# Optimization experiments

Hardware: AMD Instinct MI355X
Metric: run time of the kernel (lower is better)

## Reference

```python
import jax, jax.numpy as jnp
import numpy as np

HIDDEN = 128
N_LAYERS = 6
N_NODES = 50000
N_EDGES = 640000


def _glorot(key, shape):
    fan_in, fan_out = shape[0], shape[1]
    lim = (6.0 / (fan_in + fan_out)) ** 0.5
    return jax.random.uniform(key, shape, jnp.float32, -lim, lim)


def setup_inputs() -> dict:
    key = jax.random.key(0)
    ks = jax.random.split(key, 8)
    pos = jax.random.normal(ks[0], (N_NODES, 3), jnp.float32)
    edge_attr = jax.random.normal(ks[1], (N_EDGES, 3), jnp.float32)
    edge_index = jax.random.randint(ks[2], (2, N_EDGES), 0, N_NODES, jnp.int64)
    enc_w = _glorot(ks[3], (3, HIDDEN)); enc_b = jnp.zeros((HIDDEN,), jnp.float32)
    dec_w = _glorot(ks[4], (HIDDEN, 3)); dec_b = jnp.zeros((3,), jnp.float32)
    lk = jax.random.split(ks[5], 4 * N_LAYERS)
    edge_w1 = jnp.stack([_glorot(lk[4 * i + 0], (3 * HIDDEN, HIDDEN)) for i in range(N_LAYERS)])
    edge_w2 = jnp.stack([_glorot(lk[4 * i + 1], (HIDDEN, HIDDEN)) for i in range(N_LAYERS)])
    node_w1 = jnp.stack([_glorot(lk[4 * i + 2], (2 * HIDDEN, HIDDEN)) for i in range(N_LAYERS)])
    node_w2 = jnp.stack([_glorot(lk[4 * i + 3], (HIDDEN, HIDDEN)) for i in range(N_LAYERS)])
    edge_b1 = jnp.zeros((N_LAYERS, HIDDEN), jnp.float32)
    edge_b2 = jnp.zeros((N_LAYERS, HIDDEN), jnp.float32)
    node_b1 = jnp.zeros((N_LAYERS, HIDDEN), jnp.float32)
    node_b2 = jnp.zeros((N_LAYERS, HIDDEN), jnp.float32)
    return dict(pos=pos, edge_attr=edge_attr, edge_index=edge_index,
                enc_w=enc_w, enc_b=enc_b, dec_w=dec_w, dec_b=dec_b,
                edge_w1=edge_w1, edge_b1=edge_b1, edge_w2=edge_w2, edge_b2=edge_b2,
                node_w1=node_w1, node_b1=node_b1, node_w2=node_w2, node_b2=node_b2)


def _interaction(x, ef, src, dst, ew1, eb1, ew2, eb2, nw1, nb1, nw2, nb2, n_nodes):
    # message: concat(x_i=x[dst], x_j=x[src], edge_feature) -> edge MLP
    m = jnp.concatenate([x[dst], x[src], ef], axis=-1)            # [E, 3H]
    m = jax.nn.relu(m @ ew1 + eb1) @ ew2 + eb2                     # [E, H]
    # scatter-mean by target node
    sums = jax.ops.segment_sum(m, dst, num_segments=n_nodes)      # [N, H]
    cnt = jax.ops.segment_sum(jnp.ones((m.shape[0],), m.dtype), dst, num_segments=n_nodes)
    aggr = sums / jnp.maximum(cnt, 1.0)[:, None]
    node = jnp.concatenate([x, aggr], axis=-1)                     # [N, 2H]
    node = jax.nn.relu(node @ nw1 + nb1) @ nw2 + nb2               # [N, H]
    return x + node, ef + m


def reference(pos, edge_attr, edge_index, enc_w, enc_b, dec_w, dec_b,
              edge_w1, edge_b1, edge_w2, edge_b2,
              node_w1, node_b1, node_w2, node_b2):
    n_nodes = pos.shape[0]
    src = edge_index[0]
    dst = edge_index[1]
    x = jnp.zeros((n_nodes, HIDDEN), jnp.float32)
    ef = edge_attr @ enc_w + enc_b
    for i in range(N_LAYERS):
        x, ef = _interaction(x, ef, src, dst,
                             edge_w1[i], edge_b1[i], edge_w2[i], edge_b2[i],
                             node_w1[i], node_b1[i], node_w2[i], node_b2[i], n_nodes)
    out = x @ dec_w + dec_b                                        # [N, 3]
    # F.normalize(dim=1, eps=1e-12)
    norm = jnp.linalg.norm(out, axis=1, keepdims=True)
    return out / jnp.maximum(norm, 1e-12)
```

## Files before the change

### kernel.cpp

```cpp
#include <hip/hip_runtime.h>
#include <cstdint>

#define HIDDEN  128
#define NLAYERS 6
#define NNODES  50000
#define NEDGES  640000

typedef short short8 __attribute__((ext_vector_type(8)));
typedef float f32x4  __attribute__((ext_vector_type(4)));

__device__ __forceinline__ float bf2f(unsigned short u) {
    return __uint_as_float(((unsigned int)u) << 16);
}
__device__ __forceinline__ unsigned short f2bf(float f) {
    unsigned int u = __float_as_uint(f);
    unsigned int r = u + 0x7FFFu + ((u >> 16) & 1u);
    return (unsigned short)(r >> 16);
}
__device__ __forceinline__ unsigned int pack2(float a, float b) {
    return (unsigned int)f2bf(a) | ((unsigned int)f2bf(b) << 16);
}
__device__ __forceinline__ void unpack8(uint4 v, float* f) {
    f[0] = bf2f((unsigned short)(v.x & 0xffff)); f[1] = bf2f((unsigned short)(v.x >> 16));
    f[2] = bf2f((unsigned short)(v.y & 0xffff)); f[3] = bf2f((unsigned short)(v.y >> 16));
    f[4] = bf2f((unsigned short)(v.z & 0xffff)); f[5] = bf2f((unsigned short)(v.z >> 16));
    f[6] = bf2f((unsigned short)(v.w & 0xffff)); f[7] = bf2f((unsigned short)(v.w >> 16));
}

__global__ void detect_kernel(const int* __restrict__ ei, int* __restrict__ flag)
{
    int lane = threadIdx.x;
    int v = ei[2 * lane + 1];
    unsigned long long b = __ballot(v != 0);
    if (lane == 0) *flag = (b != 0ULL) ? 1 : 0;
}

__global__ void normidx_kernel(const int* __restrict__ ei, const int* __restrict__ flag,
                               int* __restrict__ s32, int* __restrict__ d32)
{
    int e = blockIdx.x * blockDim.x + threadIdx.x;
    if (e >= NEDGES) return;
    int s, d;
    if (*flag) { s = ei[e]; d = ei[NEDGES + e]; }
    else       { s = ei[2 * e]; d = ei[2 * (NEDGES + e)]; }
    s32[e] = min(max(s, 0), NNODES - 1);
    d32[e] = min(max(d, 0), NNODES - 1);
}

__global__ void degree_kernel(const int* __restrict__ dst, int* __restrict__ deg)
{
    int e = blockIdx.x * blockDim.x + threadIdx.x;
    if (e < NEDGES) atomicAdd(&deg[dst[e]], 1);
}

#define SCAN_T 1024
__global__ void scan_kernel(const int* __restrict__ deg, int* __restrict__ off,
                            int* __restrict__ cursor)
{
    __shared__ int part[SCAN_T];
    const int t = threadIdx.x;
    const int CH = (NNODES + SCAN_T - 1) / SCAN_T;
    const int base = t * CH;
    int s = 0;
    for (int i = 0; i < CH; ++i) {
        int idx = base + i;
        if (idx < NNODES) s += deg[idx];
    }
    part[t] = s;
    __syncthreads();
    for (int d = 1; d < SCAN_T; d <<= 1) {
        int v = (t >= d) ? part[t - d] : 0;
        __syncthreads();
        part[t] += v;
        __syncthreads();
    }
    int run = (t == 0) ? 0 : part[t - 1];
    for (int i = 0; i < CH; ++i) {
        int idx = base + i;
        if (idx < NNODES) {
            off[idx] = run;
            cursor[idx] = run;
            run += deg[idx];
        }
    }
    if (t == SCAN_T - 1) off[NNODES] = run;
}

__global__ void scatter_kernel(const int* __restrict__ s32, const int* __restrict__ d32,
                               int* __restrict__ cursor,
                               int* __restrict__ sp, int* __restrict__ dp, int* __restrict__ ep)
{
    int e = blockIdx.x * blockDim.x + threadIdx.x;
    if (e >= NEDGES) return;
    int d = d32[e];
    int p = atomicAdd(&cursor[d], 1);
    sp[p] = s32[e];
    dp[p] = d;
    ep[p] = e;
}

__global__ void transpose_kernel(const float* __restrict__ W, unsigned short* __restrict__ WT,
                                 int K, int N, int L)
{
    long idx = (long)blockIdx.x * 256 + threadIdx.x;
    long tot = (long)L * K * N;
    if (idx >= tot) return;
    int kn = (int)(idx % ((long)K * N));
    int l  = (int)(idx / ((long)K * N));
    int k = kn / N;
    int n = kn % N;
    WT[(long)l * K * N + (long)n * K + k] = f2bf(W[idx]);
}

__global__ void encode_kernel(const float* __restrict__ ea,
                              const float* __restrict__ w,
                              const float* __restrict__ b,
                              const int* __restrict__ ep,
                              unsigned short* __restrict__ ef)
{
    int idx = blockIdx.x * blockDim.x + threadIdx.x;
    int p = idx >> 5;
    if (p >= NEDGES) return;
    int e = ep[p];
    int j = (idx & 31) << 2;
    float a0 = ea[e * 3 + 0], a1 = ea[e * 3 + 1], a2 = ea[e * 3 + 2];
    float4 w0 = *(const float4*)(w + 0 * HIDDEN + j);
    float4 w1 = *(const float4*)(w + 1 * HIDDEN + j);
    float4 w2 = *(const float4*)(w + 2 * HIDDEN + j);
    float4 bb = *(const float4*)(b + j);
    ushort4 o;
    o.x = f2bf(fmaf(a0, w0.x, fmaf(a1, w1.x, fmaf(a2, w2.x, bb.x))));
    o.y = f2bf(fmaf(a0, w0.y, fmaf(a1, w1.y, fmaf(a2, w2.y, bb.y))));
    o.z = f2bf(fmaf(a0, w0.z, fmaf(a1, w1.z, fmaf(a2, w2.z, bb.z))));
    o.w = f2bf(fmaf(a0, w0.w, fmaf(a1, w1.w, fmaf(a2, w2.w, bb.w))));
    *(ushort4*)(ef + (long)p * HIDDEN + j) = o;
}

__global__ __launch_bounds__(256, 3)
void edge_layer_mfma(const unsigned short* __restrict__ Xa,
                     const unsigned short* __restrict__ Xb,
                     unsigned short* __restrict__ ef,
                     float* __restrict__ sums,
                     const int* __restrict__ sp,
                     const int* __restrict__ dp,
                     const unsigned short* __restrict__ W1T,
                     const float* __restrict__ b1,
                     const unsigned short* __restrict__ W2T,
                     const float* __restrict__ b2)
{
    __shared__ __align__(16) unsigned char buf[45056];
    unsigned short* As = (unsigned short*)buf;
    unsigned short* Hs = (unsigned short*)buf;
    unsigned short* Bs = (unsigned short*)(buf + 34816);
    __shared__ int dv[128];
    __shared__ int sv[128];

    const int tid = threadIdx.x;
    const long eb = (long)blockIdx.x * 128;
    if (tid < 128) dv[tid]       = dp[eb + tid];
    else           sv[tid - 128] = sp[eb + tid - 128];

    const int lane = tid & 63;
    const int wv   = tid >> 6;
    const int mn   = lane & 15;
    const int q    = lane >> 4;
    const int rr   = tid >> 1;
    const int o    = (tid & 1) << 4;
    const int bn   = tid >> 1;
    const int bk   = (tid & 1) << 4;

    __syncthreads();

    f32x4 acc[2][8];
#pragma unroll
    for (int h = 0; h < 2; ++h)
#pragma unroll
        for (int t = 0; t < 8; ++t) acc[h][t] = (f32x4)0.0f;

    uint4 pa0, pa1, pw0, pw1;
    {
        const unsigned short* epp = ef + (eb + rr) * HIDDEN + o;
        pa0 = *(const uint4*)epp;
        pa1 = *(const uint4*)(epp + 8);
        const unsigned short* wp = W1T + (long)bn * 384 + 256 + bk;
        pw0 = *(const uint4*)wp;
        pw1 = *(const uint4*)(wp + 8);
    }

    for (int c = 0; c < 4; ++c) {
        *(uint4*)&As[rr * 40 + o]     = pa0;
        *(uint4*)&As[rr * 40 + o + 8] = pa1;
        *(uint4*)&Bs[bn * 40 + bk]     = pw0;
        *(uint4*)&Bs[bn * 40 + bk + 8] = pw1;
        __syncthreads();

        if (c + 1 < 4) {
            const int cn = c + 1;
            const unsigned short* epp = ef + (eb + rr) * HIDDEN + (cn << 5) + o;
            pa0 = *(const uint4*)epp;
            pa1 = *(const uint4*)(epp + 8);
            const unsigned short* wp = W1T + (long)bn * 384 + 256 + (cn << 5) + bk;
            pw0 = *(const uint4*)wp;
            pw1 = *(const uint4*)(wp + 8);
        }

        short8 af0 = *(short8*)&As[(wv * 32 + mn) * 40 + (q << 3)];
        short8 af1 = *(short8*)&As[(wv * 32 + 16 + mn) * 40 + (q << 3)];
#pragma unroll
        for (int nt = 0; nt < 8; ++nt) {
            short8 bf = *(short8*)&Bs[(nt * 16 + mn) * 40 + (q << 3)];
            acc[0][nt] = __builtin_amdgcn_mfma_f32_16x16x32_bf16(af0, bf, acc[0][nt], 0, 0, 0);
            acc[1][nt] = __builtin_amdgcn_mfma_f32_16x16x32_bf16(af1, bf, acc[1][nt], 0, 0, 0);
        }
        __syncthreads();
    }

#pragma unroll
    for (int h = 0; h < 2; ++h)
#pragma unroll
        for (int r = 0; r < 4; ++r) {
            const int row = wv * 32 + h * 16 + q * 4 + r;
            const long ba = (long)dv[row] * HIDDEN;
            const long bb = (long)sv[row] * HIDDEN;
#pragma unroll
            for (int nt = 0; nt < 8; ++nt) {
                const int col = nt * 16 + mn;
                float add = bf2f(Xa[ba + col]) + bf2f(Xb[bb + col]) + b1[col];
                float hv = fmaxf(acc[h][nt][r] + add, 0.0f);
                Hs[row * 136 + col] = f2bf(hv);
            }
        }

    f32x4 acc2[2][8];
#pragma unroll
    for (int h = 0; h < 2; ++h)
#pragma unroll
        for (int t = 0; t < 8; ++t) acc2[h][t] = (f32x4)0.0f;
    {
        const unsigned short* wp = W2T + (long)bn * 128 + bk;
        pw0 = *(const uint4*)wp;
        pw1 = *(const uint4*)(wp + 8);
    }
    for (int c = 0; c < 4; ++c) {
        *(uint4*)&Bs[bn * 40 + bk]     = pw0;
        *(uint4*)&Bs[bn * 40 + bk + 8] = pw1;
        __syncthreads();
        if (c + 1 < 4) {
            const unsigned short* wp = W2T + (long)bn * 128 + ((c + 1) << 5) + bk;
            pw0 = *(const uint4*)wp;
            pw1 = *(const uint4*)(wp + 8);
        }
        short8 af0 = *(short8*)&Hs[(wv * 32 + mn) * 136 + (c << 5) + (q << 3)];
        short8 af1 = *(short8*)&Hs[(wv * 32 + 16 + mn) * 136 + (c << 5) + (q << 3)];
#pragma unroll
        for (int nt = 0; nt < 8; ++nt) {
            short8 bf = *(short8*)&Bs[(nt * 16 + mn) * 40 + (q << 3)];
            acc2[0][nt] = __builtin_amdgcn_mfma_f32_16x16x32_bf16(af0, bf, acc2[0][nt], 0, 0, 0);
            acc2[1][nt] = __builtin_amdgcn_mfma_f32_16x16x32_bf16(af1, bf, acc2[1][nt], 0, 0, 0);
        }
        __syncthreads();
    }

#pragma unroll
    for (int h = 0; h < 2; ++h)
#pragma unroll
        for (int nt = 0; nt < 8; ++nt) {
            float b2v = b2[nt * 16 + mn];
#pragma unroll
            for (int r = 0; r < 4; ++r) {
                Hs[(wv * 32 + h * 16 + q * 4 + r) * 136 + nt * 16 + mn] = f2bf(acc2[h][nt][r] + b2v);
            }
        }
    __syncthreads();

    {
        const int row = tid >> 1;
        const int ch  = (tid & 1) << 6;
        unsigned short* ep_ = ef + (eb + row) * HIDDEN + ch;
        const unsigned short* hp = &Hs[row * 136 + ch];
#pragma unroll
        for (int i = 0; i < 8; ++i) {
            uint4 mh = *(uint4*)(hp + (i << 3));
            uint4 eo = *(const uint4*)(ep_ + (i << 3));
            float m[8], e[8];
            unpack8(mh, m);
            unpack8(eo, e);
            uint4 nw;
            nw.x = pack2(e[0] + m[0], e[1] + m[1]);
            nw.y = pack2(e[2] + m[2], e[3] + m[3]);
            nw.z = pack2(e[4] + m[4], e[5] + m[5]);
            nw.w = pack2(e[6] + m[6], e[7] + m[7]);
            *(uint4*)(ep_ + (i << 3)) = nw;
        }
    }

    {
        const int cp = (tid & 63) << 1;
        const int qr = tid >> 6;
        float s0 = 0.0f, s1 = 0.0f;
        int cur = dv[qr * 32];
        for (int r = 0; r < 32; ++r) {
            const int row = qr * 32 + r;
            const int d = dv[row];
            if (d != cur) {
                atomicAdd(&sums[(long)cur * HIDDEN + cp], s0);
                atomicAdd(&sums[(long)cur * HIDDEN + cp + 1], s1);
                s0 = 0.0f; s1 = 0.0f;
                cur = d;
            }
            unsigned int u = *(unsigned int*)&Hs[row * 136 + cp];
            s0 += bf2f((unsigned short)(u & 0xffff));
            s1 += bf2f((unsigned short)(u >> 16));
        }
        atomicAdd(&sums[(long)cur * HIDDEN + cp], s0);
        atomicAdd(&sums[(long)cur * HIDDEN + cp + 1], s1);
    }
}

__global__ __launch_bounds__(256, 4)
void node_layer_mfma(float* __restrict__ x,
                     float* __restrict__ sums,
                     const int* __restrict__ deg,
                     const unsigned short* __restrict__ N1T,
                     const float* __restrict__ b1,
                     const unsigned short* __restrict__ N2T,
                     const float* __restrict__ b2,
                     const unsigned short* __restrict__ W1Tn,
                     unsigned short* __restrict__ Xa,
                     unsigned short* __restrict__ Xb)
{
    __shared__ __align__(16) unsigned short As[64 * 40];
    __shared__ __align__(16) unsigned short Bs[128 * 40];
    __shared__ __align__(16) unsigned short Hs[64 * 136];
    __shared__ float cInv[64];

    const int tid = threadIdx.x;
    const long n0 = (long)blockIdx.x * 64;
    if (tid < 64) {
        long n = n0 + tid;
        cInv[tid] = (n < NNODES) ? 1.0f / fmaxf((float)deg[n], 1.0f) : 0.0f;
    }

    const int lane = tid & 63;
    const int wv   = tid >> 6;
    const int mn   = lane & 15;
    const int q    = lane >> 4;
    const int srow = tid >> 2;
    const int sseg = tid & 3;
    const int bn   = tid >> 1;
    const int bk   = (tid & 1) << 4;

    long nr = n0 + srow;
    if (nr >= NNODES) nr = NNODES - 1;

    __syncthreads();

    f32x4 acc[8];
#pragma unroll
    for (int t = 0; t < 8; ++t) acc[t] = (f32x4)0.0f;

    float4 pa0, pa1;
    uint4 pb0, pb1;
    {
        const float* spx = x + nr * HIDDEN + (sseg << 3);
        pa0 = *(const float4*)spx;
        pa1 = *(const float4*)(spx + 4);
        const unsigned short* wp = N1T + (long)bn * 256 + bk;
        pb0 = *(const uint4*)wp;
        pb1 = *(const uint4*)(wp + 8);
    }
    float scCur = 1.0f;
    for (int c = 0; c < 8; ++c) {
        {
            uint4 w;
            w.x = pack2(pa0.x * scCur, pa0.y * scCur); w.y = pack2(pa0.z * scCur, pa0.w * scCur);
            w.z = pack2(pa1.x * scCur, pa1.y * scCur); w.w = pack2(pa1.z * scCur, pa1.w * scCur);
            *(uint4*)&As[srow * 40 + (sseg << 3)] = w;
        }
        *(uint4*)&Bs[bn * 40 + bk]     = pb0;
        *(uint4*)&Bs[bn * 40 + bk + 8] = pb1;
        __syncthreads();
        if (c + 1 < 8) {
            const int cn = c + 1;
            const float* base = (cn < 4) ? x : sums;
            scCur = (cn < 4) ? 1.0f : cInv[srow];
            const float* spx = base + nr * HIDDEN + ((cn & 3) << 5) + (sseg << 3);
            pa0 = *(const float4*)spx;
            pa1 = *(const float4*)(spx + 4);
            const unsigned short* wp = N1T + (long)bn * 256 + (cn << 5) + bk;
            pb0 = *(const uint4*)wp;
            pb1 = *(const uint4*)(wp + 8);
        }
        short8 af = *(short8*)&As[(wv * 16 + mn) * 40 + (q << 3)];
#pragma unroll
        for (int nt = 0; nt < 8; ++nt) {
            short8 bf = *(short8*)&Bs[(nt * 16 + mn) * 40 + (q << 3)];
            acc[nt] = __builtin_amdgcn_mfma_f32_16x16x32_bf16(af, bf, acc[nt], 0, 0, 0);
        }
        __syncthreads();
    }

    {
        long row = n0 + srow;
        if (row < NNODES) {
            float4 z = make_float4(0.f, 0.f, 0.f, 0.f);
            float* p = sums + row * HIDDEN + (sseg << 5);
#pragma unroll
            for (int i = 0; i < 8; ++i) ((float4*)p)[i] = z;
        }
    }

#pragma unroll
    for (int nt = 0; nt < 8; ++nt) {
        float b1v = b1[nt * 16 + mn];
#pragma unroll
        for (int r = 0; r < 4; ++r) {
            float hv = fmaxf(acc[nt][r] + b1v, 0.0f);
            Hs[(wv * 16 + q * 4 + r) * 136 + nt * 16 + mn] = f2bf(hv);
        }
    }

    f32x4 acc2[8];
#pragma unroll
    for (int t = 0; t < 8; ++t) acc2[t] = (f32x4)0.0f;
    {
        const unsigned short* wp = N2T + (long)bn * 128 + bk;
        pb0 = *(const uint4*)wp;
        pb1 = *(const uint4*)(wp + 8);
    }
    for (int c = 0; c < 4; ++c) {
        *(uint4*)&Bs[bn * 40 + bk]     = pb0;
        *(uint4*)&Bs[bn * 40 + bk + 8] = pb1;
        __syncthreads();
        if (c + 1 < 4) {
            const unsigned short* wp = N2T + (long)bn * 128 + ((c + 1) << 5) + bk;
            pb0 = *(const uint4*)wp;
            pb1 = *(const uint4*)(wp + 8);
        }
        short8 af = *(short8*)&Hs[(wv * 16 + mn) * 136 + (c << 5) + (q << 3)];
#pragma unroll
        for (int nt = 0; nt < 8; ++nt) {
            short8 bf = *(short8*)&Bs[(nt * 16 + mn) * 40 + (q << 3)];
            acc2[nt] = __builtin_amdgcn_mfma_f32_16x16x32_bf16(af, bf, acc2[nt], 0, 0, 0);
        }
        __syncthreads();
    }

#pragma unroll
    for (int nt = 0; nt < 8; ++nt) {
        float b2v = b2[nt * 16 + mn];
#pragma unroll
        for (int r = 0; r < 4; ++r) {
            long row = n0 + wv * 16 + q * 4 + r;
            float xn = 0.0f;
            if (row < NNODES) {
                float* p = x + row * HIDDEN + nt * 16 + mn;
                xn = *p + acc2[nt][r] + b2v;
                *p = xn;
            }
            Hs[(wv * 16 + q * 4 + r) * 136 + nt * 16 + mn] = f2bf(xn);
        }
    }

    if (W1Tn) {
#pragma unroll
        for (int half = 0; half < 2; ++half) {
            f32x4 accN[8];
#pragma unroll
            for (int t = 0; t < 8; ++t) accN[t] = (f32x4)0.0f;
            const int kbase = half << 7;
            {
                const unsigned short* wp = W1Tn + (long)bn * 384 + kbase + bk;
                pb0 = *(const uint4*)wp;
                pb1 = *(const uint4*)(wp + 8);
            }
            for (int c = 0; c < 4; ++c) {
                *(uint4*)&Bs[bn * 40 + bk]     = pb0;
                *(uint4*)&Bs[bn * 40 + bk + 8] = pb1;
                __syncthreads();
                if (c + 1 < 4) {
                    const unsigned short* wp = W1Tn + (long)bn * 384 + kbase + ((c + 1) << 5) + bk;
                    pb0 = *(const uint4*)wp;
                    pb1 = *(const uint4*)(wp + 8);
                }
                short8 af = *(short8*)&Hs[(wv * 16 + mn) * 136 + (c << 5) + (q << 3)];
#pragma unroll
                for (int nt = 0; nt < 8; ++nt) {
                    short8 bf = *(short8*)&Bs[(nt * 16 + mn) * 40 + (q << 3)];
                    accN[nt] = __builtin_amdgcn_mfma_f32_16x16x32_bf16(af, bf, accN[nt], 0, 0, 0);
                }
                __syncthreads();
            }
            unsigned short* Xout = half ? Xb : Xa;
#pragma unroll
            for (int nt = 0; nt < 8; ++nt) {
#pragma unroll
                for (int r = 0; r < 4; ++r) {
                    long row = n0 + wv * 16 + q * 4 + r;
                    if (row < NNODES) {
                        Xout[row * HIDDEN + nt * 16 + mn] = f2bf(accN[nt][r]);
                    }
                }
            }
        }
    }
}

__global__ void decode_kernel(const float* __restrict__ x,
                              const float* __restrict__ w,
                              const float* __restrict__ b,
                              float* __restrict__ out)
{
    int gid = blockIdx.x * blockDim.x + threadIdx.x;
    int node = gid >> 6;
    int lane = threadIdx.x & 63;
    if (node >= NNODES) return;
    float a0 = 0.f, a1 = 0.f, a2 = 0.f;
#pragma unroll
    for (int k = lane; k < HIDDEN; k += 64) {
        float xv = x[(long)node * HIDDEN + k];
        a0 = fmaf(xv, w[k * 3 + 0], a0);
        a1 = fmaf(xv, w[k * 3 + 1], a1);
        a2 = fmaf(xv, w[k * 3 + 2], a2);
    }
#pragma unroll
    for (int off = 32; off > 0; off >>= 1) {
        a0 += __shfl_down(a0, off);
        a1 += __shfl_down(a1, off);
        a2 += __shfl_down(a2, off);
    }
    if (lane == 0) {
        a0 += b[0]; a1 += b[1]; a2 += b[2];
        float nrm = sqrtf(a0 * a0 + a1 * a1 + a2 * a2);
        float inv = 1.0f / fmaxf(nrm, 1e-12f);
        out[(long)node * 3 + 0] = a0 * inv;
        out[(long)node * 3 + 1] = a1 * inv;
        out[(long)node * 3 + 2] = a2 * inv;
    }
}

extern "C" void kernel_launch(void* const* d_in, const int* in_sizes, int n_in,
                              void* d_out, int out_size, void* d_ws, size_t ws_size,
                              hipStream_t stream)
{
    const float* edge_attr = (const float*)d_in[1];
    const int*   ei        = (const int*)d_in[2];
    const float* enc_w     = (const float*)d_in[3];
    const float* enc_b     = (const float*)d_in[4];
    const float* dec_w     = (const float*)d_in[5];
    const float* dec_b     = (const float*)d_in[6];
    const float* edge_w1   = (const float*)d_in[7];
    const float* edge_b1   = (const float*)d_in[8];
    const float* edge_w2   = (const float*)d_in[9];
    const float* edge_b2   = (const float*)d_in[10];
    const float* node_w1   = (const float*)d_in[11];
    const float* node_b1   = (const float*)d_in[12];
    const float* node_w2   = (const float*)d_in[13];
    const float* node_b2   = (const float*)d_in[14];

    char* ws = (char*)d_ws;
    unsigned short* ef  = (unsigned short*)(ws);
    float* x      = (float*)(ws + 163840000L);
    float* sums   = (float*)(ws + 189440000L);
    int*   src32  = (int*)  (ws + 215040000L);
    int*   dst32  = (int*)  (ws + 217600000L);
    int*   sp     = (int*)  (ws + 220160000L);
    int*   dp     = (int*)  (ws + 222720000L);
    int*   eperm  = (int*)  (ws + 225280000L);
    int*   deg    = (int*)  (ws + 227840000L);
    int*   off    = (int*)  (ws + 228040704L);
    int*   cursor = (int*)  (ws + 228241408L);
    int*   flag   = (int*)  (ws + 228442112L);
    unsigned short* W1T = (unsigned short*)(ws + 228442176L);
    unsigned short* W2T = (unsigned short*)(ws + 229032000L);
    unsigned short* N1T = (unsigned short*)(ws + 229228608L);
    unsigned short* N2T = (unsigned short*)(ws + 229621824L);
    unsigned short* Xa  = (unsigned short*)(ws + 229818432L);
    unsigned short* Xb  = (unsigned short*)(ws + 242618432L);

    float* out = (float*)d_out;

    hipMemsetAsync(x, 0, (size_t)NNODES * HIDDEN * sizeof(float), stream);
    hipMemsetAsync(sums, 0, (size_t)NNODES * HIDDEN * sizeof(float), stream);
    hipMemsetAsync(deg, 0, 200704, stream);
    hipMemsetAsync(Xa, 0, 25600000, stream);

    detect_kernel<<<1, 64, 0, stream>>>(ei, flag);
    normidx_kernel<<<(NEDGES + 255) / 256, 256, 0, stream>>>(ei, flag, src32, dst32);
    degree_kernel<<<(NEDGES + 255) / 256, 256, 0, stream>>>(dst32, deg);
    scan_kernel<<<1, SCAN_T, 0, stream>>>(deg, off, cursor);
    scatter_kernel<<<(NEDGES + 255) / 256, 256, 0, stream>>>(src32, dst32, cursor, sp, dp, eperm);
    encode_kernel<<<(NEDGES * 32 + 255) / 256, 256, 0, stream>>>(edge_attr, enc_w, enc_b, eperm, ef);

    transpose_kernel<<<(6 * 384 * 128 + 255) / 256, 256, 0, stream>>>(edge_w1, W1T, 384, 128, 6);
    transpose_kernel<<<(6 * 128 * 128 + 255) / 256, 256, 0, stream>>>(edge_w2, W2T, 128, 128, 6);
    transpose_kernel<<<(6 * 256 * 128 + 255) / 256, 256, 0, stream>>>(node_w1, N1T, 256, 128, 6);
    transpose_kernel<<<(6 * 128 * 128 + 255) / 256, 256, 0, stream>>>(node_w2, N2T, 128, 128, 6);

    for (int l = 0; l < NLAYERS; ++l) {
        edge_layer_mfma<<<NEDGES / 128, 256, 0, stream>>>(
            Xa, Xb, ef, sums, sp, dp,
            W1T + (long)l * 384 * 128, edge_b1 + (long)l * HIDDEN,
            W2T + (long)l * 128 * 128, edge_b2 + (long)l * HIDDEN);
        const unsigned short* w1next = (l + 1 < NLAYERS) ? (W1T + (long)(l + 1) * 384 * 128) : nullptr;
        node_layer_mfma<<<(NNODES + 63) / 64, 256, 0, stream>>>(
            x, sums, deg,
            N1T + (long)l * 256 * 128, node_b1 + (long)l * HIDDEN,
            N2T + (long)l * 128 * 128, node_b2 + (long)l * HIDDEN,
            w1next, Xa, Xb);
    }

    decode_kernel<<<(NNODES * 64 + 255) / 256, 256, 0, stream>>>(x, dec_w, dec_b, out);
}
```

Baseline: 1.683 ms.

## Load MFMA operands directly from global memory instead of staging through LDS

The edge and node MFMA kernels now read A and B fragments straight from global memory, where the weights are small and cache-resident. This drops the shared-memory staging buffers and most per-chunk barriers. Shared memory shrinks to the Hs buffer, so the edge kernel's launch bounds rise from 3 to 4 blocks per CU. The cost is more global and L2 traffic for weight fragments and less explicit load/compute overlap. The zeroing of sums in the node kernel moves to the end.

Result: slower. 2.958 ms (+75.8%).

```diff
diff --git a/kernel.cpp b/kernel.cpp
--- a/kernel.cpp
+++ b/kernel.cpp
@@ -136,7 +136,7 @@
     *(ushort4*)(ef + (long)p * HIDDEN + j) = o;
 }
 
-__global__ __launch_bounds__(256, 3)
+__global__ __launch_bounds__(256, 4)
 void edge_layer_mfma(const unsigned short* __restrict__ Xa,
                      const unsigned short* __restrict__ Xb,
                      unsigned short* __restrict__ ef,
@@ -148,10 +148,7 @@
                      const unsigned short* __restrict__ W2T,
                      const float* __restrict__ b2)
 {
-    __shared__ __align__(16) unsigned char buf[45056];
-    unsigned short* As = (unsigned short*)buf;
-    unsigned short* Hs = (unsigned short*)buf;
-    unsigned short* Bs = (unsigned short*)(buf + 34816);
+    __shared__ __align__(16) unsigned short Hs[128 * 136];
     __shared__ int dv[128];
     __shared__ int sv[128];
 
@@ -164,56 +161,30 @@
     const int wv   = tid >> 6;
     const int mn   = lane & 15;
     const int q    = lane >> 4;
-    const int rr   = tid >> 1;
-    const int o    = (tid & 1) << 4;
-    const int bn   = tid >> 1;
-    const int bk   = (tid & 1) << 4;
-
+
+    f32x4 acc[2][8];
+#pragma unroll
+    for (int h = 0; h < 2; ++h)
+#pragma unroll
+        for (int t = 0; t < 8; ++t) acc[h][t] = (f32x4)0.0f;
+
+    {
+        const unsigned short* a0p = ef + (eb + wv * 32 + mn) * HIDDEN + (q << 3);
+        const unsigned short* a1p = a0p + 16 * HIDDEN;
+        const unsigned short* bp  = W1T + (long)mn * 384 + 256 + (q << 3);
+#pragma unroll
+        for (int c = 0; c < 4; ++c) {
+            short8 af0 = *(const short8*)(a0p + (c << 5));
+            short8 af1 = *(const short8*)(a1p + (c << 5));
+#pragma unroll
+            for (int nt = 0; nt < 8; ++nt) {
+                short8 bf = *(const short8*)(bp + (long)nt * (16 * 384) + (c << 5));
+                acc[0][nt] = __builtin_amdgcn_mfma_f32_16x16x32_bf16(af0, bf, acc[0][nt], 0, 0, 0);
+                acc[1][nt] = __builtin_amdgcn_mfma_f32_16x16x32_bf16(af1, bf, acc[1][nt], 0, 0, 0);
+            }
+        }
+    }
     __syncthreads();
-
-    f32x4 acc[2][8];
-#pragma unroll
-    for (int h = 0; h < 2; ++h)
-#pragma unroll
-        for (int t = 0; t < 8; ++t) acc[h][t] = (f32x4)0.0f;
-
-    uint4 pa0, pa1, pw0, pw1;
-    {
-        const unsigned short* epp = ef + (eb + rr) * HIDDEN + o;
-        pa0 = *(const uint4*)epp;
-        pa1 = *(const uint4*)(epp + 8);
-        const unsigned short* wp = W1T + (long)bn * 384 + 256 + bk;
-        pw0 = *(const uint4*)wp;
-        pw1 = *(const uint4*)(wp + 8);
-    }
-
-    for (int c = 0; c < 4; ++c) {
-        *(uint4*)&As[rr * 40 + o]     = pa0;
-        *(uint4*)&As[rr * 40 + o + 8] = pa1;
-        *(uint4*)&Bs[bn * 40 + bk]     = pw0;
-        *(uint4*)&Bs[bn * 40 + bk + 8] = pw1;
-        __syncthreads();
-
-        if (c + 1 < 4) {
-            const int cn = c + 1;
-            const unsigned short* epp = ef + (eb + rr) * HIDDEN + (cn << 5) + o;
-            pa0 = *(const uint4*)epp;
-            pa1 = *(const uint4*)(epp + 8);
-            const unsigned short* wp = W1T + (long)bn * 384 + 256 + (cn << 5) + bk;
-            pw0 = *(const uint4*)wp;
-            pw1 = *(const uint4*)(wp + 8);
-        }
-
-        short8 af0 = *(short8*)&As[(wv * 32 + mn) * 40 + (q << 3)];
-        short8 af1 = *(short8*)&As[(wv * 32 + 16 + mn) * 40 + (q << 3)];
-#pragma unroll
-        for (int nt = 0; nt < 8; ++nt) {
-            short8 bf = *(short8*)&Bs[(nt * 16 + mn) * 40 + (q << 3)];
-            acc[0][nt] = __builtin_amdgcn_mfma_f32_16x16x32_bf16(af0, bf, acc[0][nt], 0, 0, 0);
-            acc[1][nt] = __builtin_amdgcn_mfma_f32_16x16x32_bf16(af1, bf, acc[1][nt], 0, 0, 0);
-        }
-        __syncthreads();
-    }
 
 #pragma unroll
     for (int h = 0; h < 2; ++h)
@@ -230,6 +201,7 @@
                 Hs[row * 136 + col] = f2bf(hv);
             }
         }
+    __syncthreads();
 
     f32x4 acc2[2][8];
 #pragma unroll
@@ -237,28 +209,20 @@
 #pragma unroll
         for (int t = 0; t < 8; ++t) acc2[h][t] = (f32x4)0.0f;
     {
-        const unsigned short* wp = W2T + (long)bn * 128 + bk;
-        pw0 = *(const uint4*)wp;
-        pw1 = *(const uint4*)(wp + 8);
-    }
-    for (int c = 0; c < 4; ++c) {
-        *(uint4*)&Bs[bn * 40 + bk]     = pw0;
-        *(uint4*)&Bs[bn * 40 + bk + 8] = pw1;
-        __syncthreads();
-        if (c + 1 < 4) {
-            const unsigned short* wp = W2T + (long)bn * 128 + ((c + 1) << 5) + bk;
-            pw0 = *(const uint4*)wp;
-            pw1 = *(const uint4*)(wp + 8);
-        }
-        short8 af0 = *(short8*)&Hs[(wv * 32 + mn) * 136 + (c << 5) + (q << 3)];
-        short8 af1 = *(short8*)&Hs[(wv * 32 + 16 + mn) * 136 + (c << 5) + (q << 3)];
-#pragma unroll
-        for (int nt = 0; nt < 8; ++nt) {
-            short8 bf = *(short8*)&Bs[(nt * 16 + mn) * 40 + (q << 3)];
-            acc2[0][nt] = __builtin_amdgcn_mfma_f32_16x16x32_bf16(af0, bf, acc2[0][nt], 0, 0, 0);
-            acc2[1][nt] = __builtin_amdgcn_mfma_f32_16x16x32_bf16(af1, bf, acc2[1][nt], 0, 0, 0);
-        }
-        __syncthreads();
+        const unsigned short* h0p = &Hs[(wv * 32 + mn) * 136 + (q << 3)];
+        const unsigned short* h1p = h0p + 16 * 136;
+        const unsigned short* bp  = W2T + (long)mn * 128 + (q << 3);
+#pragma unroll
+        for (int c = 0; c < 4; ++c) {
+            short8 af0 = *(const short8*)(h0p + (c << 5));
+            short8 af1 = *(const short8*)(h1p + (c << 5));
+#pragma unroll
+            for (int nt = 0; nt < 8; ++nt) {
+                short8 bf = *(const short8*)(bp + nt * (16 * 128) + (c << 5));
+                acc2[0][nt] = __builtin_amdgcn_mfma_f32_16x16x32_bf16(af0, bf, acc2[0][nt], 0, 0, 0);
+                acc2[1][nt] = __builtin_amdgcn_mfma_f32_16x16x32_bf16(af1, bf, acc2[1][nt], 0, 0, 0);
+            }
+        }
     }
 
 #pragma unroll
@@ -329,84 +293,39 @@
                      unsigned short* __restrict__ Xa,
                      unsigned short* __restrict__ Xb)
 {
-    __shared__ __align__(16) unsigned short As[64 * 40];
-    __shared__ __align__(16) unsigned short Bs[128 * 40];
     __shared__ __align__(16) unsigned short Hs[64 * 136];
-    __shared__ float cInv[64];
 
     const int tid = threadIdx.x;
     const long n0 = (long)blockIdx.x * 64;
-    if (tid < 64) {
-        long n = n0 + tid;
-        cInv[tid] = (n < NNODES) ? 1.0f / fmaxf((float)deg[n], 1.0f) : 0.0f;
-    }
-
     const int lane = tid & 63;
     const int wv   = tid >> 6;
     const int mn   = lane & 15;
     const int q    = lane >> 4;
-    const int srow = tid >> 2;
-    const int sseg = tid & 3;
-    const int bn   = tid >> 1;
-    const int bk   = (tid & 1) << 4;
-
-    long nr = n0 + srow;
-    if (nr >= NNODES) nr = NNODES - 1;
-
-    __syncthreads();
+
+    long arow = n0 + wv * 16 + mn;
+    if (arow >= NNODES) arow = NNODES - 1;
+    const float cInvL = 1.0f / fmaxf((float)deg[arow], 1.0f);
 
     f32x4 acc[8];
 #pragma unroll
     for (int t = 0; t < 8; ++t) acc[t] = (f32x4)0.0f;
 
-    float4 pa0, pa1;
-    uint4 pb0, pb1;
-    {
-        const float* spx = x + nr * HIDDEN + (sseg << 3);
-        pa0 = *(const float4*)spx;
-        pa1 = *(const float4*)(spx + 4);
-        const unsigned short* wp = N1T + (long)bn * 256 + bk;
-        pb0 = *(const uint4*)wp;
-        pb1 = *(const uint4*)(wp + 8);
-    }
-    float scCur = 1.0f;
+#pragma unroll
     for (int c = 0; c < 8; ++c) {
-        {
-            uint4 w;
-            w.x = pack2(pa0.x * scCur, pa0.y * scCur); w.y = pack2(pa0.z * scCur, pa0.w * scCur);
-            w.z = pack2(pa1.x * scCur, pa1.y * scCur); w.w = pack2(pa1.z * scCur, pa1.w * scCur);
-            *(uint4*)&As[srow * 40 + (sseg << 3)] = w;
-        }
-        *(uint4*)&Bs[bn * 40 + bk]     = pb0;
-        *(uint4*)&Bs[bn * 40 + bk + 8] = pb1;
-        __syncthreads();
-        if (c + 1 < 8) {
-            const int cn = c + 1;
-            const float* base = (cn < 4) ? x : sums;
-            scCur = (cn < 4) ? 1.0f : cInv[srow];
-            const float* spx = base + nr * HIDDEN + ((cn & 3) << 5) + (sseg << 3);
-            pa0 = *(const float4*)spx;
-            pa1 = *(const float4*)(spx + 4);
-            const unsigned short* wp = N1T + (long)bn * 256 + (cn << 5) + bk;
-            pb0 = *(const uint4*)wp;
-            pb1 = *(const uint4*)(wp + 8);
-        }
-        short8 af = *(short8*)&As[(wv * 16 + mn) * 40 + (q << 3)];
+        const float* base = (c < 4) ? (x + arow * HIDDEN + (c << 5))
+                                    : (sums + arow * HIDDEN + ((c - 4) << 5));
+        const float sc = (c < 4) ? 1.0f : cInvL;
+        float4 v0 = *(const float4*)(base + (q << 3));
+        float4 v1 = *(const float4*)(base + (q << 3) + 4);
+        uint4 u;
+        u.x = pack2(v0.x * sc, v0.y * sc); u.y = pack2(v0.z * sc, v0.w * sc);
+        u.z = pack2(v1.x * sc, v1.y * sc); u.w = pack2(v1.z * sc, v1.w * sc);
+        short8 af = *(short8*)&u;
+        const unsigned short* bp = N1T + (long)mn * 256 + (c << 5) + (q << 3);
 #pragma unroll
         for (int nt = 0; nt < 8; ++nt) {
-            short8 bf = *(short8*)&Bs[(nt * 16 + mn) * 40 + (q << 3)];
+            short8 bf = *(const short8*)(bp + nt * (16 * 256));
             acc[nt] = __builtin_amdgcn_mfma_f32_16x16x32_bf16(af, bf, acc[nt], 0, 0, 0);
-        }
-        __syncthreads();
-    }
-
-    {
-        long row = n0 + srow;
-        if (row < NNODES) {
-            float4 z = make_float4(0.f, 0.f, 0.f, 0.f);
-            float* p = sums + row * HIDDEN + (sseg << 5);
-#pragma unroll
-            for (int i = 0; i < 8; ++i) ((float4*)p)[i] = z;
         }
     }
 
@@ -419,31 +338,23 @@
             Hs[(wv * 16 + q * 4 + r) * 136 + nt * 16 + mn] = f2bf(hv);
         }
     }
+    __syncthreads();
 
     f32x4 acc2[8];
 #pragma unroll
     for (int t = 0; t < 8; ++t) acc2[t] = (f32x4)0.0f;
     {
-        const unsigned short* wp = N2T + (long)bn * 128 + bk;
-        pb0 = *(const uint4*)wp;
-        pb1 = *(const uint4*)(wp + 8);
-    }
-    for (int c = 0; c < 4; ++c) {
-        *(uint4*)&Bs[bn * 40 + bk]     = pb0;
-        *(uint4*)&Bs[bn * 40 + bk + 8] = pb1;
-        __syncthreads();
-        if (c + 1 < 4) {
-            const unsigned short* wp = N2T + (long)bn * 128 + ((c + 1) << 5) + bk;
-            pb0 = *(const uint4*)wp;
-            pb1 = *(const uint4*)(wp + 8);
-        }
-        short8 af = *(short8*)&Hs[(wv * 16 + mn) * 136 + (c << 5) + (q << 3)];
-#pragma unroll
-        for (int nt = 0; nt < 8; ++nt) {
-            short8 bf = *(short8*)&Bs[(nt * 16 + mn) * 40 + (q << 3)];
-            acc2[nt] = __builtin_amdgcn_mfma_f32_16x16x32_bf16(af, bf, acc2[nt], 0, 0, 0);
-        }
-        __syncthreads();
+        const unsigned short* hp = &Hs[(wv * 16 + mn) * 136 + (q << 3)];
+        const unsigned short* bp = N2T + (long)mn * 128 + (q << 3);
+#pragma unroll
+        for (int c = 0; c < 4; ++c) {
+            short8 af = *(const short8*)(hp + (c << 5));
+#pragma unroll
+            for (int nt = 0; nt < 8; ++nt) {
+                short8 bf = *(const short8*)(bp + nt * (16 * 128) + (c << 5));
+                acc2[nt] = __builtin_amdgcn_mfma_f32_16x16x32_bf16(af, bf, acc2[nt], 0, 0, 0);
+            }
+        }
     }
 
 #pragma unroll
@@ -461,6 +372,7 @@
             Hs[(wv * 16 + q * 4 + r) * 136 + nt * 16 + mn] = f2bf(xn);
         }
     }
+    __syncthreads();
 
     if (W1Tn) {
 #pragma unroll
@@ -468,28 +380,16 @@
             f32x4 accN[8];
 #pragma unroll
             for (int t = 0; t < 8; ++t) accN[t] = (f32x4)0.0f;
-            const int kbase = half << 7;
-            {
-                const unsigned short* wp = W1Tn + (long)bn * 384 + kbase + bk;
-                pb0 = *(const uint4*)wp;
-                pb1 = *(const uint4*)(wp + 8);
-            }
+            const unsigned short* hp = &Hs[(wv * 16 + mn) * 136 + (q << 3)];
+            const unsigned short* bp = W1Tn + (long)mn * 384 + (half << 7) + (q << 3);
+#pragma unroll
             for (int c = 0; c < 4; ++c) {
-                *(uint4*)&Bs[bn * 40 + bk]     = pb0;
-                *(uint4*)&Bs[bn * 40 + bk + 8] = pb1;
-                __syncthreads();
-                if (c + 1 < 4) {
-                    const unsigned short* wp = W1Tn + (long)bn * 384 + kbase + ((c + 1) << 5) + bk;
-                    pb0 = *(const uint4*)wp;
-                    pb1 = *(const uint4*)(wp + 8);
-                }
-                short8 af = *(short8*)&Hs[(wv * 16 + mn) * 136 + (c << 5) + (q << 3)];
+                short8 af = *(const short8*)(hp + (c << 5));
 #pragma unroll
                 for (int nt = 0; nt < 8; ++nt) {
-                    short8 bf = *(short8*)&Bs[(nt * 16 + mn) * 40 + (q << 3)];
+                    short8 bf = *(const short8*)(bp + (long)nt * (16 * 384) + (c << 5));
                     accN[nt] = __builtin_amdgcn_mfma_f32_16x16x32_bf16(af, bf, accN[nt], 0, 0, 0);
                 }
-                __syncthreads();
             }
             unsigned short* Xout = half ? Xb : Xa;
 #pragma unroll
@@ -502,6 +402,18 @@
                     }
                 }
             }
+        }
+    }
+
+    {
+        const int srow = tid >> 2;
+        const int sseg = tid & 3;
+        long row = n0 + srow;
+        if (row < NNODES) {
+            float4 z = make_float4(0.f, 0.f, 0.f, 0.f);
+            float* p = sums + row * HIDDEN + (sseg << 5);
+#pragma unroll
+            for (int i = 0; i < 8; ++i) ((float4*)p)[i] = z;
         }
     }
 }
```

## Vectorize node-feature gathers and reuse edge-feature fragments from registers

Applied to the files above, without the earlier changes.

The first-GEMM epilogue previously did scalar 2-byte gathers of Xa[dst] and Xb[src] per accumulator element. Now the raw accumulator is staged in shared memory, and each lane then gathers contiguous 16-byte chunks of a whole row to apply bias and ReLU. The edge-feature A fragments already loaded for the first GEMM are kept in registers and reused for the residual update, so edge features are not re-read from global memory. Two block barriers are dropped, since each wave now only touches its own rows. This raises register pressure and depends on per-wave row ownership being correct.

Measured after the change: 1.544 ms. 8.2% less time.

```diff
diff --git a/kernel.cpp b/kernel.cpp
--- a/kernel.cpp
+++ b/kernel.cpp
@@ -169,13 +169,13 @@
     const int bn   = tid >> 1;
     const int bk   = (tid & 1) << 4;
 
-    __syncthreads();
-
     f32x4 acc[2][8];
 #pragma unroll
     for (int h = 0; h < 2; ++h)
 #pragma unroll
         for (int t = 0; t < 8; ++t) acc[h][t] = (f32x4)0.0f;
+
+    short8 efold0[4], efold1[4];
 
     uint4 pa0, pa1, pw0, pw1;
     {
@@ -188,8 +188,8 @@
     }
 
     for (int c = 0; c < 4; ++c) {
-        *(uint4*)&As[rr * 40 + o]     = pa0;
-        *(uint4*)&As[rr * 40 + o + 8] = pa1;
+        *(uint4*)&As[rr * 40 + o]      = pa0;
+        *(uint4*)&As[rr * 40 + o + 8]  = pa1;
         *(uint4*)&Bs[bn * 40 + bk]     = pw0;
         *(uint4*)&Bs[bn * 40 + bk + 8] = pw1;
         __syncthreads();
@@ -206,6 +206,8 @@
 
         short8 af0 = *(short8*)&As[(wv * 32 + mn) * 40 + (q << 3)];
         short8 af1 = *(short8*)&As[(wv * 32 + 16 + mn) * 40 + (q << 3)];
+        efold0[c] = af0;
+        efold1[c] = af1;
 #pragma unroll
         for (int nt = 0; nt < 8; ++nt) {
             short8 bf = *(short8*)&Bs[(nt * 16 + mn) * 40 + (q << 3)];
@@ -218,18 +220,39 @@
 #pragma unroll
     for (int h = 0; h < 2; ++h)
 #pragma unroll
-        for (int r = 0; r < 4; ++r) {
-            const int row = wv * 32 + h * 16 + q * 4 + r;
-            const long ba = (long)dv[row] * HIDDEN;
-            const long bb = (long)sv[row] * HIDDEN;
-#pragma unroll
-            for (int nt = 0; nt < 8; ++nt) {
-                const int col = nt * 16 + mn;
-                float add = bf2f(Xa[ba + col]) + bf2f(Xb[bb + col]) + b1[col];
-                float hv = fmaxf(acc[h][nt][r] + add, 0.0f);
-                Hs[row * 136 + col] = f2bf(hv);
-            }
-        }
+        for (int nt = 0; nt < 8; ++nt)
+#pragma unroll
+            for (int r = 0; r < 4; ++r)
+                Hs[(wv * 32 + h * 16 + q * 4 + r) * 136 + nt * 16 + mn] = f2bf(acc[h][nt][r]);
+
+    {
+        const int row  = wv * 32 + (lane >> 1);
+        const int ch   = (lane & 1) << 6;
+        const unsigned short* xap = Xa + (long)dv[row] * HIDDEN + ch;
+        const unsigned short* xbp = Xb + (long)sv[row] * HIDDEN + ch;
+        unsigned short* hp = &Hs[row * 136 + ch];
+#pragma unroll
+        for (int i = 0; i < 8; ++i) {
+            uint4 va = *(const uint4*)(xap + (i << 3));
+            uint4 vb = *(const uint4*)(xbp + (i << 3));
+            uint4 vp = *(uint4*)(hp + (i << 3));
+            float fa[8], fb[8], fp[8];
+            unpack8(va, fa); unpack8(vb, fb); unpack8(vp, fp);
+            const float* bp = b1 + ch + (i << 3);
+            uint4 nw;
+            float h0 = fmaxf(fp[0] + fa[0] + fb[0] + bp[0], 0.0f);
+            float h1 = fmaxf(fp[1] + fa[1] + fb[1] + bp[1], 0.0f);
+            float h2 = fmaxf(fp[2] + fa[2] + fb[2] + bp[2], 0.0f);
+            float h3 = fmaxf(fp[3] + fa[3] + fb[3] + bp[3], 0.0f);
+            float h4 = fmaxf(fp[4] + fa[4] + fb[4] + bp[4], 0.0f);
+            float h5 = fmaxf(fp[5] + fa[5] + fb[5] + bp[5], 0.0f);
+            float h6 = fmaxf(fp[6] + fa[6] + fb[6] + bp[6], 0.0f);
+            float h7 = fmaxf(fp[7] + fa[7] + fb[7] + bp[7], 0.0f);
+            nw.x = pack2(h0, h1); nw.y = pack2(h2, h3);
+            nw.z = pack2(h4, h5); nw.w = pack2(h6, h7);
+            *(uint4*)(hp + (i << 3)) = nw;
+        }
+    }
 
     f32x4 acc2[2][8];
 #pragma unroll
@@ -267,30 +290,28 @@
         for (int nt = 0; nt < 8; ++nt) {
             float b2v = b2[nt * 16 + mn];
 #pragma unroll
-            for (int r = 0; r < 4; ++r) {
+            for (int r = 0; r < 4; ++r)
                 Hs[(wv * 32 + h * 16 + q * 4 + r) * 136 + nt * 16 + mn] = f2bf(acc2[h][nt][r] + b2v);
-            }
-        }
-    __syncthreads();
-
-    {
-        const int row = tid >> 1;
-        const int ch  = (tid & 1) << 6;
-        unsigned short* ep_ = ef + (eb + row) * HIDDEN + ch;
-        const unsigned short* hp = &Hs[row * 136 + ch];
-#pragma unroll
-        for (int i = 0; i < 8; ++i) {
-            uint4 mh = *(uint4*)(hp + (i << 3));
-            uint4 eo = *(const uint4*)(ep_ + (i << 3));
+        }
+
+#pragma unroll
+    for (int h = 0; h < 2; ++h) {
+        const int row = wv * 32 + h * 16 + mn;
+        unsigned short* ep_ = ef + (eb + row) * HIDDEN + (q << 3);
+#pragma unroll
+        for (int c = 0; c < 4; ++c) {
+            uint4 mh = *(uint4*)&Hs[row * 136 + (c << 5) + (q << 3)];
             float m[8], e[8];
             unpack8(mh, m);
-            unpack8(eo, e);
+            short8 eo = h ? efold1[c] : efold0[c];
+            uint4 eu = *(uint4*)&eo;
+            unpack8(eu, e);
             uint4 nw;
             nw.x = pack2(e[0] + m[0], e[1] + m[1]);
             nw.y = pack2(e[2] + m[2], e[3] + m[3]);
             nw.z = pack2(e[4] + m[4], e[5] + m[5]);
             nw.w = pack2(e[6] + m[6], e[7] + m[7]);
-            *(uint4*)(ep_ + (i << 3)) = nw;
+            *(uint4*)(ep_ + (c << 5)) = nw;
         }
     }
 
```
